# Optimization experiments

Measured on AMD Instinct MI355X. Metric: run time of the kernel, lower is better.

The kernel has to match this reference:

```python
import jax, jax.numpy as jnp
import numpy as np

N = 100000
E = 2000000
F = 64          # in_features == out_features (required by attention * h_j)
BETA = 0.5
NEG_SLOPE = 0.01  # torch F.leaky_relu default


def setup_inputs() -> dict:
    key = jax.random.key(0)
    k1, k2, k3, k4, k5, k6 = jax.random.split(key, 6)
    h = jax.random.normal(k1, (N, F), dtype=jnp.float32)
    adj = jax.random.randint(k2, (2, E), 0, N, dtype=jnp.int64)
    amount = jax.random.uniform(k3, (E,), dtype=jnp.float32)
    count = jax.random.uniform(k4, (E,), dtype=jnp.float32)
    fc_w = jax.random.normal(k5, (F, 2 * F), dtype=jnp.float32) * (1.0 / np.sqrt(2 * F))
    fc_b = jax.random.normal(k6, (F,), dtype=jnp.float32) * 0.01
    return {"h": h, "adj": adj, "amount": amount, "count": count,
            "fc_w": fc_w, "fc_b": fc_b}


def _minmax_norm(x):
    lo, hi = x.min(), x.max()
    return (x - lo) / (hi - lo + 1e-8)


def reference(h, adj, amount, count, fc_w, fc_b):
    # per-edge weight from normalized amount/count
    edge_weight = BETA * _minmax_norm(amount) + (1.0 - BETA) * _minmax_norm(count)  # [E]

    src, dst = adj[0], adj[1]
    h_i = h[src]                     # [E, F]
    h_j = h[dst]                     # [E, F]
    h_cat = jnp.concatenate([h_i, h_j], axis=1)  # [E, 2F]

    score = jnp.einsum('ef,of->eo', h_cat, fc_w) + fc_b  # [E, F_out]
    score = jnp.where(score >= 0, score, NEG_SLOPE * score)  # leaky_relu
    score = score * edge_weight[:, None]

    # softmax over ALL edges (dim 0), per feature, as in the original
    attention = jax.nn.softmax(score, axis=0)  # [E, F]

    agg = jnp.zeros_like(h).at[src].add(attention * h_j)  # scatter-add -> [N, F]
    return agg
```

## Files before the change

kernel.cpp:

```cpp
#include <hip/hip_runtime.h>
#include <hip/hip_fp16.h>
#include <math.h>

#define FDIM   64
#define NB     64
#define BSHIFT 7
#define BMASK  127
#define EPTA   16
#define CHUNKA (EPTA * 256)
#define SCH    1024
#define CAP    3072

__global__ __launch_bounds__(256) void count_mm_k(const int* __restrict__ src,
                                                  const float* __restrict__ amount,
                                                  const float* __restrict__ count,
                                                  int* __restrict__ mat,
                                                  float4* __restrict__ partial,
                                                  double* __restrict__ colsum,
                                                  int E, int nblkA, int nbkt) {
  __shared__ int lhist[1024];
  __shared__ float4 lred[4];
  for (int k = threadIdx.x; k < nbkt; k += 256) lhist[k] = 0;
  if (blockIdx.x == 0)
    for (int i = threadIdx.x; i < 1024; i += 256) colsum[i] = 0.0;
  __syncthreads();
  float amin = 3.4e38f, amax = -3.4e38f, cmin = 3.4e38f, cmax = -3.4e38f;
  int e0 = blockIdx.x * CHUNKA + threadIdx.x * EPTA;
  if (e0 + EPTA <= E) {
    #pragma unroll
    for (int q = 0; q < EPTA; q += 4) {
      int4   s4 = *(const int4*)(src + e0 + q);
      float4 a4 = *(const float4*)(amount + e0 + q);
      float4 c4 = *(const float4*)(count + e0 + q);
      atomicAdd(&lhist[s4.x >> BSHIFT], 1);
      atomicAdd(&lhist[s4.y >> BSHIFT], 1);
      atomicAdd(&lhist[s4.z >> BSHIFT], 1);
      atomicAdd(&lhist[s4.w >> BSHIFT], 1);
      amin = fminf(amin, fminf(fminf(a4.x, a4.y), fminf(a4.z, a4.w)));
      amax = fmaxf(amax, fmaxf(fmaxf(a4.x, a4.y), fmaxf(a4.z, a4.w)));
      cmin = fminf(cmin, fminf(fminf(c4.x, c4.y), fminf(c4.z, c4.w)));
      cmax = fmaxf(cmax, fmaxf(fmaxf(c4.x, c4.y), fmaxf(c4.z, c4.w)));
    }
  } else {
    for (int e = e0; e < E; e++) {
      atomicAdd(&lhist[src[e] >> BSHIFT], 1);
      float a = amount[e], c = count[e];
      amin = fminf(amin, a); amax = fmaxf(amax, a);
      cmin = fminf(cmin, c); cmax = fmaxf(cmax, c);
    }
  }
  #pragma unroll
  for (int off = 32; off; off >>= 1) {
    amin = fminf(amin, __shfl_down(amin, off));
    amax = fmaxf(amax, __shfl_down(amax, off));
    cmin = fminf(cmin, __shfl_down(cmin, off));
    cmax = fmaxf(cmax, __shfl_down(cmax, off));
  }
  if ((threadIdx.x & 63) == 0) lred[threadIdx.x >> 6] = make_float4(amin, amax, cmin, cmax);
  __syncthreads();
  for (int k = threadIdx.x; k < nbkt; k += 256)
    mat[(size_t)k * nblkA + blockIdx.x] = lhist[k];
  if (threadIdx.x == 0) {
    float4 r = lred[0];
    #pragma unroll
    for (int w = 1; w < 4; w++) {
      r.x = fminf(r.x, lred[w].x); r.y = fmaxf(r.y, lred[w].y);
      r.z = fminf(r.z, lred[w].z); r.w = fmaxf(r.w, lred[w].w);
    }
    partial[blockIdx.x] = r;
  }
}

__global__ __launch_bounds__(256) void scan1_k(const int* __restrict__ v,
                                               int* __restrict__ bsum, int M) {
  __shared__ int lds[256];
  int t = threadIdx.x, b = blockIdx.x;
  int s = 0;
  for (int i = b * SCH + t; i < min((b + 1) * SCH, M); i += 256) s += v[i];
  lds[t] = s; __syncthreads();
  for (int off = 128; off; off >>= 1) {
    if (t < off) lds[t] += lds[t + off];
    __syncthreads();
  }
  if (t == 0) bsum[b] = lds[0];
}

__global__ __launch_bounds__(256) void scan2_k(const int* __restrict__ bsum,
                                               int* __restrict__ bexcl, int nchunk,
                                               const float4* __restrict__ partial,
                                               float* __restrict__ mmf, int nb) {
  __shared__ int lds[256];
  int t = threadIdx.x;
  int running = 0;
  for (int c0 = 0; c0 < nchunk; c0 += 256) {
    int x = (c0 + t < nchunk) ? bsum[c0 + t] : 0;
    lds[t] = x; __syncthreads();
    for (int off = 1; off < 256; off <<= 1) {
      int v = (t >= off) ? lds[t - off] : 0;
      __syncthreads();
      lds[t] += v; __syncthreads();
    }
    if (c0 + t < nchunk) bexcl[c0 + t] = running + lds[t] - x;
    running += lds[255];
    __syncthreads();
  }
  float amin = 3.4e38f, amax = -3.4e38f, cmin = 3.4e38f, cmax = -3.4e38f;
  for (int i = t; i < nb; i += 256) {
    float4 p = partial[i];
    amin = fminf(amin, p.x); amax = fmaxf(amax, p.y);
    cmin = fminf(cmin, p.z); cmax = fmaxf(cmax, p.w);
  }
  #pragma unroll
  for (int off = 32; off; off >>= 1) {
    amin = fminf(amin, __shfl_down(amin, off));
    amax = fmaxf(amax, __shfl_down(amax, off));
    cmin = fminf(cmin, __shfl_down(cmin, off));
    cmax = fmaxf(cmax, __shfl_down(cmax, off));
  }
  __shared__ float4 lred[4];
  if ((t & 63) == 0) lred[t >> 6] = make_float4(amin, amax, cmin, cmax);
  __syncthreads();
  if (t == 0) {
    float4 r = lred[0];
    #pragma unroll
    for (int w = 1; w < 4; w++) {
      r.x = fminf(r.x, lred[w].x); r.y = fmaxf(r.y, lred[w].y);
      r.z = fminf(r.z, lred[w].z); r.w = fmaxf(r.w, lred[w].w);
    }
    mmf[0] = r.x; mmf[1] = r.y; mmf[2] = r.z; mmf[3] = r.w;
  }
}

__global__ __launch_bounds__(256) void scan3_k(const int* __restrict__ v,
                                               const int* __restrict__ bexcl,
                                               int* __restrict__ smat, int M) {
  __shared__ int lds[256];
  int t = threadIdx.x, b = blockIdx.x;
  int running = bexcl[b];
  for (int tile = 0; tile < SCH; tile += 256) {
    int i = b * SCH + tile + t;
    int x = (i < M) ? v[i] : 0;
    lds[t] = x; __syncthreads();
    for (int off = 1; off < 256; off <<= 1) {
      int vv = (t >= off) ? lds[t - off] : 0;
      __syncthreads();
      lds[t] += vv; __syncthreads();
    }
    if (i < M) smat[i] = running + lds[t] - x;
    running += lds[255];
    __syncthreads();
  }
}

__global__ __launch_bounds__(256) void scatter_k(const int* __restrict__ src,
                                                 const int* __restrict__ dst,
                                                 const float* __restrict__ amount,
                                                 const float* __restrict__ count,
                                                 const float* __restrict__ mmf,
                                                 const int* __restrict__ smat,
                                                 int2* __restrict__ payload,
                                                 int E, int nblkA, int nbkt) {
  __shared__ int cntb[1024];
  __shared__ int baseb[1024];
  __shared__ int sbase[1024];
  __shared__ int wsum[4];
  __shared__ int2 lpay[CHUNKA];
  __shared__ unsigned short lbkt[CHUNKA];
  const int t = threadIdx.x, blk = blockIdx.x;
  for (int k = t; k < nbkt; k += 256) {
    cntb[k] = 0;
    sbase[k] = smat[(size_t)k * nblkA + blk];
  }
  __syncthreads();
  const float amin = mmf[0], amax = mmf[1], cmin = mmf[2], cmax = mmf[3];
  const float L2E = 1.4426950408889634f;
  const float ascale = 0.5f * L2E / (amax - amin + 1e-8f);
  const float cscale = 0.5f * L2E / (cmax - cmin + 1e-8f);
  int e0 = blk * CHUNKA + t * EPTA;
  const bool full = (e0 + EPTA <= E);
  int4 S[4]; int4 D[4]; float4 A[4]; float4 C[4];
  if (full) {
    #pragma unroll
    for (int q = 0; q < 4; q++) {
      S[q] = *(const int4*)(src + e0 + 4 * q);
      D[q] = *(const int4*)(dst + e0 + 4 * q);
      A[q] = *(const float4*)(amount + e0 + 4 * q);
      C[q] = *(const float4*)(count + e0 + 4 * q);
      atomicAdd(&cntb[S[q].x >> BSHIFT], 1);
      atomicAdd(&cntb[S[q].y >> BSHIFT], 1);
      atomicAdd(&cntb[S[q].z >> BSHIFT], 1);
      atomicAdd(&cntb[S[q].w >> BSHIFT], 1);
    }
  } else {
    for (int e = e0; e < E; e++) atomicAdd(&cntb[src[e] >> BSHIFT], 1);
  }
  __syncthreads();
  {
    const int wv = t >> 6, ln = t & 63;
    int carry = 0;
    #pragma unroll
    for (int c = 0; c < 4; c++) {
      int idx = (wv << 8) + (c << 6) + ln;
      int x = (idx < nbkt) ? cntb[idx] : 0;
      int v = x;
      #pragma unroll
      for (int off = 1; off < 64; off <<= 1) {
        int u = __shfl_up(v, off);
        if (ln >= off) v += u;
      }
      if (idx < nbkt) baseb[idx] = carry + v - x;
      carry += __shfl(v, 63);
    }
    if (ln == 0) wsum[wv] = carry;
  }
  __syncthreads();
  {
    const int wv = t >> 6, ln = t & 63;
    int wpre = 0;
    #pragma unroll
    for (int i = 0; i < 4; i++) wpre += (i < wv) ? wsum[i] : 0;
    if (wpre) {
      #pragma unroll
      for (int c = 0; c < 4; c++) {
        int idx = (wv << 8) + (c << 6) + ln;
        if (idx < nbkt) baseb[idx] += wpre;
      }
    }
  }
  __syncthreads();
  for (int k = t; k < nbkt; k += 256) cntb[k] = baseb[k];
  __syncthreads();
  auto ins = [&](int s, int d, float a, float c) {
    int b = s >> BSHIFT;
    float ew = (a - amin) * ascale + (c - cmin) * cscale;
    int pos = atomicAdd(&cntb[b], 1);
    lpay[pos] = make_int2((d << 8) | (s & BMASK), __float_as_int(ew));
    lbkt[pos] = (unsigned short)b;
  };
  if (full) {
    #pragma unroll
    for (int q = 0; q < 4; q++) {
      ins(S[q].x, D[q].x, A[q].x, C[q].x);
      ins(S[q].y, D[q].y, A[q].y, C[q].y);
      ins(S[q].z, D[q].z, A[q].z, C[q].z);
      ins(S[q].w, D[q].w, A[q].w, C[q].w);
    }
  } else {
    for (int e = e0; e < E; e++) ins(src[e], dst[e], amount[e], count[e]);
  }
  __syncthreads();
  const int ned = min(CHUNKA, E - blk * CHUNKA);
  for (int i = t; i < ned; i += 256) {
    int bk = lbkt[i];
    payload[sbase[bk] + (i - baseb[bk])] = lpay[i];
  }
}

__global__ __launch_bounds__(128) void pre_gemm(const float* __restrict__ h,
                                                const float* __restrict__ fc_w,
                                                const float* __restrict__ fc_b,
                                                float* __restrict__ G1,
                                                __half2* __restrict__ P, int N) {
  __shared__ float hs[NB * FDIM];
  const int t = threadIdx.x;
  const int o = t & 63, half = t >> 6;
  float w[FDIM];
  const float* wrow = fc_w + o * 128 + half * 64;
  #pragma unroll
  for (int f = 0; f < FDIM; f += 4) {
    float4 v = *(const float4*)(wrow + f);
    w[f] = v.x; w[f + 1] = v.y; w[f + 2] = v.z; w[f + 3] = v.w;
  }
  const float bias = (half == 0) ? fc_b[o] : 0.0f;
  const int n0 = blockIdx.x * NB;
  const int nrows = min(NB, N - n0);
  for (int i = t; i < nrows * FDIM; i += 128) hs[i] = h[(size_t)n0 * FDIM + i];
  __syncthreads();
  for (int n = 0; n < nrows; n++) {
    float4 a4 = make_float4(0.f, 0.f, 0.f, 0.f);
    #pragma unroll
    for (int f = 0; f < FDIM; f += 4) {
      float4 hv = *(const float4*)(&hs[n * FDIM + f]);
      a4.x += hv.x * w[f];
      a4.y += hv.y * w[f + 1];
      a4.z += hv.z * w[f + 2];
      a4.w += hv.w * w[f + 3];
    }
    float acc = (a4.x + a4.y) + (a4.z + a4.w) + bias;
    if (half == 0) {
      G1[(size_t)(n0 + n) * FDIM + o] = acc;
    } else {
      P[(size_t)(n0 + n) * FDIM + o] =
          __halves2half2(__float2half(acc), __float2half(hs[n * FDIM + o]));
    }
  }
}

__device__ __forceinline__ float2 unpack_h2(unsigned u) {
  __half2 v = *(__half2*)&u;
  return make_float2(__low2float(v), __high2float(v));
}

__global__ __launch_bounds__(512) void fusedB_k(const int2* __restrict__ payload,
                                                const int* __restrict__ smat,
                                                const float* __restrict__ G1,
                                                const unsigned* __restrict__ P,
                                                double* __restrict__ colsum,
                                                float* __restrict__ out,
                                                int E, int nblkA, int nbkt) {
  __shared__ int2 lpay[CAP];
  __shared__ int fcnt[128];
  __shared__ int fcur[128];
  __shared__ float part[512];
  const int b = blockIdx.x;
  const int t = threadIdx.x;
  const int lane = t & 63;
  const int wv = __builtin_amdgcn_readfirstlane(t >> 6);
  const int node0 = b << BSHIFT;
  const int base = smat[(size_t)b * nblkA];
  const int end  = (b + 1 < nbkt) ? smat[(size_t)(b + 1) * nblkA] : E;
  const int nchunks = (end - base + CAP - 1) / CAP;
  const bool multi = (nchunks > 1);
  float csum = 0.0f;
  for (int c = 0; c < nchunks; c++) {
    const int cs = base + c * CAP;
    const int m = min(CAP, end - cs);
    if (t < 128) fcnt[t] = 0;
    __syncthreads();
    int2 myp0, myp1, myp2, myp3, myp4, myp5;
    {
      int i;
      i = t;            if (i < m) { myp0 = payload[cs + i]; atomicAdd(&fcnt[myp0.x & 127], 1); }
      i = t + 512;      if (i < m) { myp1 = payload[cs + i]; atomicAdd(&fcnt[myp1.x & 127], 1); }
      i = t + 1024;     if (i < m) { myp2 = payload[cs + i]; atomicAdd(&fcnt[myp2.x & 127], 1); }
      i = t + 1536;     if (i < m) { myp3 = payload[cs + i]; atomicAdd(&fcnt[myp3.x & 127], 1); }
      i = t + 2048;     if (i < m) { myp4 = payload[cs + i]; atomicAdd(&fcnt[myp4.x & 127], 1); }
      i = t + 2560;     if (i < m) { myp5 = payload[cs + i]; atomicAdd(&fcnt[myp5.x & 127], 1); }
    }
    __syncthreads();
    if (wv == 0) {
      int carry = 0;
      #pragma unroll
      for (int cc = 0; cc < 2; cc++) {
        int idx = (cc << 6) + lane;
        int x = fcnt[idx];
        int v = x;
        #pragma unroll
        for (int off = 1; off < 64; off <<= 1) {
          int u = __shfl_up(v, off);
          if (lane >= off) v += u;
        }
        fcur[idx] = carry + v - x;
        carry += __shfl(v, 63);
      }
    }
    __syncthreads();
    {
      int i;
      i = t;            if (i < m) lpay[atomicAdd(&fcur[myp0.x & 127], 1)] = myp0;
      i = t + 512;      if (i < m) lpay[atomicAdd(&fcur[myp1.x & 127], 1)] = myp1;
      i = t + 1024;     if (i < m) lpay[atomicAdd(&fcur[myp2.x & 127], 1)] = myp2;
      i = t + 1536;     if (i < m) lpay[atomicAdd(&fcur[myp3.x & 127], 1)] = myp3;
      i = t + 2048;     if (i < m) lpay[atomicAdd(&fcur[myp4.x & 127], 1)] = myp4;
      i = t + 2560;     if (i < m) lpay[atomicAdd(&fcur[myp5.x & 127], 1)] = myp5;
    }
    __syncthreads();
    const int per = (((m + 7) >> 3) + 63) & ~63;
    const int ws = wv * per;
    const int we = min(ws + per, m);
    int curnode = -1;
    bool firstf = true;
    float acc = 0.0f, g1 = 0.0f;
    auto flush_to = [&](int node) {
      if (curnode >= 0) {
        float* dp = out + (size_t)curnode * FDIM + lane;
        if (multi || firstf) { atomicAdd(dp, acc); firstf = false; }
        else *dp = acc;
      }
      curnode = node; acc = 0.0f;
      g1 = G1[(size_t)node * FDIM + lane];
    };
    for (int c0 = ws; c0 < we; c0 += 64) {
      const int mm = min(64, we - c0);
      int2 p = make_int2(0, 0);
      if (lane < mm) p = lpay[c0 + lane];
      if (mm == 64) {
        #pragma unroll 1
        for (int j = 0; j < 64; j += 16) {
          int xs[16]; float ee[16]; unsigned uu[16];
          #pragma unroll
          for (int k = 0; k < 16; k++) {
            xs[k] = __builtin_amdgcn_readlane(p.x, j + k);
            ee[k] = __int_as_float(__builtin_amdgcn_readlane(p.y, j + k));
          }
          #pragma unroll
          for (int k = 0; k < 16; k++) {
            unsigned off = (((unsigned)xs[k]) & 0xFFFFFF00u) | ((unsigned)lane << 2);
            uu[k] = *(const unsigned*)((const char*)P + off);
          }
          #pragma unroll
          for (int k = 0; k < 16; k++) {
            int node = node0 + (xs[k] & 127);
            if (node != curnode) flush_to(node);
            float2 v = unpack_h2(uu[k]);
            float sc = g1 + v.x;
            sc = fmaxf(sc, 0.01f * sc);
            float x = exp2f(sc * ee[k]);
            csum += x;
            acc += x * v.y;
          }
        }
      } else {
        for (int j = 0; j < mm; j += 16) {
          const int rem = mm - j;
          int xs[16]; float ee[16]; unsigned uu[16];
          #pragma unroll
          for (int k = 0; k < 16; k++) {
            xs[k] = __builtin_amdgcn_readlane(p.x, j + k);
            ee[k] = __int_as_float(__builtin_amdgcn_readlane(p.y, j + k));
          }
          #pragma unroll
          for (int k = 0; k < 16; k++) {
            unsigned off = (((unsigned)xs[k]) & 0xFFFFFF00u) | ((unsigned)lane << 2);
            uu[k] = *(const unsigned*)((const char*)P + off);
          }
          #pragma unroll
          for (int k = 0; k < 16; k++) {
            if (k < rem) {
              int node = node0 + (xs[k] & 127);
              if (node != curnode) flush_to(node);
              float2 v = unpack_h2(uu[k]);
              float sc = g1 + v.x;
              sc = fmaxf(sc, 0.01f * sc);
              float x = exp2f(sc * ee[k]);
              csum += x;
              acc += x * v.y;
            }
          }
        }
      }
    }
    if (curnode >= 0) atomicAdd(out + (size_t)curnode * FDIM + lane, acc);
  }
  part[t] = csum;
  __syncthreads();
  if (t < 64) {
    float tot = 0.0f;
    #pragma unroll
    for (int w = 0; w < 8; w++) tot += part[t + (w << 6)];
    atomicAdd(&colsum[t * 16], (double)tot);
  }
}

__global__ __launch_bounds__(256) void scale_k(float4* __restrict__ out4,
                                               const double* __restrict__ colsum,
                                               int total4) {
  __shared__ float rinv_s[64];
  if (threadIdx.x < 64) rinv_s[threadIdx.x] = (float)(1.0 / colsum[threadIdx.x * 16]);
  __syncthreads();
  const float4* r4 = (const float4*)rinv_s;
  int idx = blockIdx.x * blockDim.x + threadIdx.x;
  int stride = gridDim.x * blockDim.x;
  for (int i = idx; i < total4; i += stride) {
    float4 v = out4[i];
    float4 r = r4[i & 15];
    v.x *= r.x; v.y *= r.y; v.z *= r.z; v.w *= r.w;
    out4[i] = v;
  }
}

extern "C" void kernel_launch(void* const* d_in, const int* in_sizes, int n_in,
                              void* d_out, int out_size, void* d_ws, size_t ws_size,
                              hipStream_t stream) {
  const float* h      = (const float*)d_in[0];
  const int*   adj    = (const int*)d_in[1];
  const float* amount = (const float*)d_in[2];
  const float* count  = (const float*)d_in[3];
  const float* fc_w   = (const float*)d_in[4];
  const float* fc_b   = (const float*)d_in[5];
  float* out = (float*)d_out;

  const int E = in_sizes[2];
  const int N = in_sizes[0] / FDIM;
  const int* src = adj;
  const int* dst = adj + E;
  const int nbkt  = (N + BMASK) >> BSHIFT;
  const int nblkA = (E + CHUNKA - 1) / CHUNKA;
  const int M = nbkt * nblkA;
  const int nchunk = (M + SCH - 1) / SCH;

  char* ws = (char*)d_ws;
  size_t off = 0;
  auto alloc = [&](size_t bytes) { void* p = ws + off; off += (bytes + 255) & ~(size_t)255; return p; };
  float*    G1      = (float*)alloc((size_t)N * FDIM * sizeof(float));
  __half2*  P       = (__half2*)alloc((size_t)N * FDIM * sizeof(__half2));
  int2*     payload = (int2*)alloc((size_t)E * sizeof(int2));
  int*      mat     = (int*)alloc((size_t)M * sizeof(int));
  int*      smat    = (int*)alloc((size_t)M * sizeof(int));
  int*      bsum    = (int*)alloc((size_t)nchunk * sizeof(int));
  int*      bexcl   = (int*)alloc((size_t)nchunk * sizeof(int));
  float4*   mmpart  = (float4*)alloc((size_t)nblkA * sizeof(float4));
  double*   colsum  = (double*)alloc(1024 * sizeof(double));
  float*    mmf     = (float*)alloc(4 * sizeof(float));

  hipMemsetAsync(d_out, 0, (size_t)out_size * sizeof(float), stream);
  count_mm_k<<<nblkA, 256, 0, stream>>>(src, amount, count, mat, mmpart, colsum, E, nblkA, nbkt);
  scan1_k<<<nchunk, 256, 0, stream>>>(mat, bsum, M);
  scan2_k<<<1, 256, 0, stream>>>(bsum, bexcl, nchunk, mmpart, mmf, nblkA);
  scan3_k<<<nchunk, 256, 0, stream>>>(mat, bexcl, smat, M);
  scatter_k<<<nblkA, 256, 0, stream>>>(src, dst, amount, count, mmf, smat, payload, E, nblkA, nbkt);
  pre_gemm<<<(N + NB - 1) / NB, 128, 0, stream>>>(h, fc_w, fc_b, G1, P, N);
  fusedB_k<<<nbkt, 512, 0, stream>>>(payload, smat, G1, (const unsigned*)P, colsum, out, E, nblkA, nbkt);
  scale_k<<<1024, 256, 0, stream>>>((float4*)out, colsum, N * FDIM / 4);
}
```

Measured before the change: 291.3 us.

## Split each node bucket into quarters and use a persistent grid in fused aggregation

The fused aggregation kernel now splits each 128-node bucket's edge segment into four sub-ranges. These are processed as work items by a fixed grid of 2048 blocks of 256 threads, with smaller LDS chunks of 1024 edges. The aim is better load balance and occupancy than one 512-thread block per bucket (about 782 blocks), whose tails could serialize. In exchange, every flush to an output row is now an atomicAdd, since several blocks can touch the same node. There is also extra per-item sort overhead.

```diff
diff --git a/kernel.cpp b/kernel.cpp
--- a/kernel.cpp
+++ b/kernel.cpp
@@ -9,7 +9,9 @@
 #define EPTA   16
 #define CHUNKA (EPTA * 256)
 #define SCH    1024
-#define CAP    3072
+#define CAPW   1024
+#define SPLIT  4
+#define FB_GRID 2048
 
 __global__ __launch_bounds__(256) void count_mm_k(const int* __restrict__ src,
                                                   const float* __restrict__ amount,
@@ -301,132 +303,100 @@
   return make_float2(__low2float(v), __high2float(v));
 }
 
-__global__ __launch_bounds__(512) void fusedB_k(const int2* __restrict__ payload,
+__global__ __launch_bounds__(256) void fusedB_k(const int2* __restrict__ payload,
                                                 const int* __restrict__ smat,
                                                 const float* __restrict__ G1,
                                                 const unsigned* __restrict__ P,
                                                 double* __restrict__ colsum,
                                                 float* __restrict__ out,
-                                                int E, int nblkA, int nbkt) {
-  __shared__ int2 lpay[CAP];
+                                                int E, int nblkA, int nbkt,
+                                                int nitems) {
+  __shared__ int2 lpay[CAPW];
   __shared__ int fcnt[128];
   __shared__ int fcur[128];
-  __shared__ float part[512];
-  const int b = blockIdx.x;
+  __shared__ float part[256];
   const int t = threadIdx.x;
   const int lane = t & 63;
   const int wv = __builtin_amdgcn_readfirstlane(t >> 6);
-  const int node0 = b << BSHIFT;
-  const int base = smat[(size_t)b * nblkA];
-  const int end  = (b + 1 < nbkt) ? smat[(size_t)(b + 1) * nblkA] : E;
-  const int nchunks = (end - base + CAP - 1) / CAP;
-  const bool multi = (nchunks > 1);
   float csum = 0.0f;
-  for (int c = 0; c < nchunks; c++) {
-    const int cs = base + c * CAP;
-    const int m = min(CAP, end - cs);
-    if (t < 128) fcnt[t] = 0;
-    __syncthreads();
-    int2 myp0, myp1, myp2, myp3, myp4, myp5;
-    {
-      int i;
-      i = t;            if (i < m) { myp0 = payload[cs + i]; atomicAdd(&fcnt[myp0.x & 127], 1); }
-      i = t + 512;      if (i < m) { myp1 = payload[cs + i]; atomicAdd(&fcnt[myp1.x & 127], 1); }
-      i = t + 1024;     if (i < m) { myp2 = payload[cs + i]; atomicAdd(&fcnt[myp2.x & 127], 1); }
-      i = t + 1536;     if (i < m) { myp3 = payload[cs + i]; atomicAdd(&fcnt[myp3.x & 127], 1); }
-      i = t + 2048;     if (i < m) { myp4 = payload[cs + i]; atomicAdd(&fcnt[myp4.x & 127], 1); }
-      i = t + 2560;     if (i < m) { myp5 = payload[cs + i]; atomicAdd(&fcnt[myp5.x & 127], 1); }
-    }
-    __syncthreads();
-    if (wv == 0) {
-      int carry = 0;
-      #pragma unroll
-      for (int cc = 0; cc < 2; cc++) {
-        int idx = (cc << 6) + lane;
-        int x = fcnt[idx];
-        int v = x;
+  for (int w = blockIdx.x; w < nitems; w += gridDim.x) {
+    const int b = w >> 2, q = w & 3;
+    const int base = smat[(size_t)b * nblkA];
+    const int end  = (b + 1 < nbkt) ? smat[(size_t)(b + 1) * nblkA] : E;
+    const int seg  = end - base;
+    const int qlen = (seg + SPLIT - 1) / SPLIT;
+    const int is = base + q * qlen;
+    const int ie = min(is + qlen, end);
+    if (is >= ie) continue;
+    const int node0 = b << BSHIFT;
+    for (int c = is; c < ie; c += CAPW) {
+      const int m = min(CAPW, ie - c);
+      if (t < 128) fcnt[t] = 0;
+      __syncthreads();
+      int2 myp0, myp1, myp2, myp3;
+      {
+        int i;
+        i = t;        if (i < m) { myp0 = payload[c + i]; atomicAdd(&fcnt[myp0.x & 127], 1); }
+        i = t + 256;  if (i < m) { myp1 = payload[c + i]; atomicAdd(&fcnt[myp1.x & 127], 1); }
+        i = t + 512;  if (i < m) { myp2 = payload[c + i]; atomicAdd(&fcnt[myp2.x & 127], 1); }
+        i = t + 768;  if (i < m) { myp3 = payload[c + i]; atomicAdd(&fcnt[myp3.x & 127], 1); }
+      }
+      __syncthreads();
+      if (wv == 0) {
+        int carry = 0;
         #pragma unroll
-        for (int off = 1; off < 64; off <<= 1) {
-          int u = __shfl_up(v, off);
-          if (lane >= off) v += u;
+        for (int cc = 0; cc < 2; cc++) {
+          int idx = (cc << 6) + lane;
+          int x = fcnt[idx];
+          int v = x;
+          #pragma unroll
+          for (int off = 1; off < 64; off <<= 1) {
+            int u = __shfl_up(v, off);
+            if (lane >= off) v += u;
+          }
+          fcur[idx] = carry + v - x;
+          carry += __shfl(v, 63);
         }
-        fcur[idx] = carry + v - x;
-        carry += __shfl(v, 63);
       }
-    }
-    __syncthreads();
-    {
-      int i;
-      i = t;            if (i < m) lpay[atomicAdd(&fcur[myp0.x & 127], 1)] = myp0;
-      i = t + 512;      if (i < m) lpay[atomicAdd(&fcur[myp1.x & 127], 1)] = myp1;
-      i = t + 1024;     if (i < m) lpay[atomicAdd(&fcur[myp2.x & 127], 1)] = myp2;
-      i = t + 1536;     if (i < m) lpay[atomicAdd(&fcur[myp3.x & 127], 1)] = myp3;
-      i = t + 2048;     if (i < m) lpay[atomicAdd(&fcur[myp4.x & 127], 1)] = myp4;
-      i = t + 2560;     if (i < m) lpay[atomicAdd(&fcur[myp5.x & 127], 1)] = myp5;
-    }
-    __syncthreads();
-    const int per = (((m + 7) >> 3) + 63) & ~63;
-    const int ws = wv * per;
-    const int we = min(ws + per, m);
-    int curnode = -1;
-    bool firstf = true;
-    float acc = 0.0f, g1 = 0.0f;
-    auto flush_to = [&](int node) {
-      if (curnode >= 0) {
-        float* dp = out + (size_t)curnode * FDIM + lane;
-        if (multi || firstf) { atomicAdd(dp, acc); firstf = false; }
-        else *dp = acc;
+      __syncthreads();
+      {
+        int i;
+        i = t;        if (i < m) lpay[atomicAdd(&fcur[myp0.x & 127], 1)] = myp0;
+        i = t + 256;  if (i < m) lpay[atomicAdd(&fcur[myp1.x & 127], 1)] = myp1;
+        i = t + 512;  if (i < m) lpay[atomicAdd(&fcur[myp2.x & 127], 1)] = myp2;
+        i = t + 768;  if (i < m) lpay[atomicAdd(&fcur[myp3.x & 127], 1)] = myp3;
       }
-      curnode = node; acc = 0.0f;
-      g1 = G1[(size_t)node * FDIM + lane];
-    };
-    for (int c0 = ws; c0 < we; c0 += 64) {
-      const int mm = min(64, we - c0);
-      int2 p = make_int2(0, 0);
-      if (lane < mm) p = lpay[c0 + lane];
-      if (mm == 64) {
-        #pragma unroll 1
-        for (int j = 0; j < 64; j += 16) {
-          int xs[16]; float ee[16]; unsigned uu[16];
-          #pragma unroll
-          for (int k = 0; k < 16; k++) {
-            xs[k] = __builtin_amdgcn_readlane(p.x, j + k);
-            ee[k] = __int_as_float(__builtin_amdgcn_readlane(p.y, j + k));
-          }
-          #pragma unroll
-          for (int k = 0; k < 16; k++) {
-            unsigned off = (((unsigned)xs[k]) & 0xFFFFFF00u) | ((unsigned)lane << 2);
-            uu[k] = *(const unsigned*)((const char*)P + off);
-          }
-          #pragma unroll
-          for (int k = 0; k < 16; k++) {
-            int node = node0 + (xs[k] & 127);
-            if (node != curnode) flush_to(node);
-            float2 v = unpack_h2(uu[k]);
-            float sc = g1 + v.x;
-            sc = fmaxf(sc, 0.01f * sc);
-            float x = exp2f(sc * ee[k]);
-            csum += x;
-            acc += x * v.y;
-          }
-        }
-      } else {
-        for (int j = 0; j < mm; j += 16) {
-          const int rem = mm - j;
-          int xs[16]; float ee[16]; unsigned uu[16];
-          #pragma unroll
-          for (int k = 0; k < 16; k++) {
-            xs[k] = __builtin_amdgcn_readlane(p.x, j + k);
-            ee[k] = __int_as_float(__builtin_amdgcn_readlane(p.y, j + k));
-          }
-          #pragma unroll
-          for (int k = 0; k < 16; k++) {
-            unsigned off = (((unsigned)xs[k]) & 0xFFFFFF00u) | ((unsigned)lane << 2);
-            uu[k] = *(const unsigned*)((const char*)P + off);
-          }
-          #pragma unroll
-          for (int k = 0; k < 16; k++) {
-            if (k < rem) {
+      __syncthreads();
+      const int per = (((m + 3) >> 2) + 63) & ~63;
+      const int ws = wv * per;
+      const int we = min(ws + per, m);
+      int curnode = -1;
+      float acc = 0.0f, g1 = 0.0f;
+      auto flush_to = [&](int node) {
+        if (curnode >= 0) atomicAdd(out + (size_t)curnode * FDIM + lane, acc);
+        curnode = node; acc = 0.0f;
+        g1 = G1[(size_t)node * FDIM + lane];
+      };
+      for (int c0 = ws; c0 < we; c0 += 64) {
+        const int mm = min(64, we - c0);
+        int2 p = make_int2(0, 0);
+        if (lane < mm) p = lpay[c0 + lane];
+        if (mm == 64) {
+          #pragma unroll 1
+          for (int j = 0; j < 64; j += 16) {
+            int xs[16]; float ee[16]; unsigned uu[16];
+            #pragma unroll
+            for (int k = 0; k < 16; k++) {
+              xs[k] = __builtin_amdgcn_readlane(p.x, j + k);
+              ee[k] = __int_as_float(__builtin_amdgcn_readlane(p.y, j + k));
+            }
+            #pragma unroll
+            for (int k = 0; k < 16; k++) {
+              unsigned off = (((unsigned)xs[k]) & 0xFFFFFF00u) | ((unsigned)lane << 2);
+              uu[k] = *(const unsigned*)((const char*)P + off);
+            }
+            #pragma unroll
+            for (int k = 0; k < 16; k++) {
               int node = node0 + (xs[k] & 127);
               if (node != curnode) flush_to(node);
               float2 v = unpack_h2(uu[k]);
@@ -437,17 +407,43 @@
               acc += x * v.y;
             }
           }
+        } else {
+          for (int j = 0; j < mm; j += 16) {
+            const int rem = mm - j;
+            int xs[16]; float ee[16]; unsigned uu[16];
+            #pragma unroll
+            for (int k = 0; k < 16; k++) {
+              xs[k] = __builtin_amdgcn_readlane(p.x, j + k);
+              ee[k] = __int_as_float(__builtin_amdgcn_readlane(p.y, j + k));
+            }
+            #pragma unroll
+            for (int k = 0; k < 16; k++) {
+              unsigned off = (((unsigned)xs[k]) & 0xFFFFFF00u) | ((unsigned)lane << 2);
+              uu[k] = *(const unsigned*)((const char*)P + off);
+            }
+            #pragma unroll
+            for (int k = 0; k < 16; k++) {
+              if (k < rem) {
+                int node = node0 + (xs[k] & 127);
+                if (node != curnode) flush_to(node);
+                float2 v = unpack_h2(uu[k]);
+                float sc = g1 + v.x;
+                sc = fmaxf(sc, 0.01f * sc);
+                float x = exp2f(sc * ee[k]);
+                csum += x;
+                acc += x * v.y;
+              }
+            }
+          }
         }
       }
-    }
-    if (curnode >= 0) atomicAdd(out + (size_t)curnode * FDIM + lane, acc);
+      if (curnode >= 0) atomicAdd(out + (size_t)curnode * FDIM + lane, acc);
+    }
   }
   part[t] = csum;
   __syncthreads();
   if (t < 64) {
-    float tot = 0.0f;
-    #pragma unroll
-    for (int w = 0; w < 8; w++) tot += part[t + (w << 6)];
+    float tot = part[t] + part[t + 64] + part[t + 128] + part[t + 192];
     atomicAdd(&colsum[t * 16], (double)tot);
   }
 }
@@ -488,6 +484,7 @@
   const int nblkA = (E + CHUNKA - 1) / CHUNKA;
   const int M = nbkt * nblkA;
   const int nchunk = (M + SCH - 1) / SCH;
+  const int nitems = nbkt * SPLIT;
 
   char* ws = (char*)d_ws;
   size_t off = 0;
@@ -510,6 +507,6 @@
   scan3_k<<<nchunk, 256, 0, stream>>>(mat, bexcl, smat, M);
   scatter_k<<<nblkA, 256, 0, stream>>>(src, dst, amount, count, mmf, smat, payload, E, nblkA, nbkt);
   pre_gemm<<<(N + NB - 1) / NB, 128, 0, stream>>>(h, fc_w, fc_b, G1, P, N);
-  fusedB_k<<<nbkt, 512, 0, stream>>>(payload, smat, G1, (const unsigned*)P, colsum, out, E, nblkA, nbkt);
+  fusedB_k<<<FB_GRID, 256, 0, stream>>>(payload, smat, G1, (const unsigned*)P, colsum, out, E, nblkA, nbkt, nitems);
   scale_k<<<1024, 256, 0, stream>>>((float4*)out, colsum, N * FDIM / 4);
 }
```

Result: slower. 306.1 us (+5.1%).

## Replace per-block bucket matrix scan with global histogram and atomic cursors

Applied to the files above, without the earlier changes.

The per-block bucket count matrix and its three-kernel prefix scan are replaced by a global bucket histogram built with atomics. A single small scan computes bucket bases, and scatter blocks now claim output ranges through atomicAdd on per-bucket cursors. Buckets are halved to 64 nodes, and the aggregation kernel runs with 256 threads and a smaller LDS staging buffer, giving more, smaller blocks. This removes two launches and the large matrix traffic. In exchange, edge order within a bucket becomes nondeterministic, and cursor contention and more bucket entries per scatter block add cost.

```diff
diff --git a/kernel.cpp b/kernel.cpp
--- a/kernel.cpp
+++ b/kernel.cpp
@@ -4,25 +4,22 @@
 
 #define FDIM   64
 #define NB     64
-#define BSHIFT 7
-#define BMASK  127
+#define BSHIFT 6
+#define BMASK  63
+#define NBKT_AL 1792
 #define EPTA   16
 #define CHUNKA (EPTA * 256)
-#define SCH    1024
-#define CAP    3072
+#define CAP    1792
 
 __global__ __launch_bounds__(256) void count_mm_k(const int* __restrict__ src,
                                                   const float* __restrict__ amount,
                                                   const float* __restrict__ count,
-                                                  int* __restrict__ mat,
+                                                  int* __restrict__ ghist,
                                                   float4* __restrict__ partial,
-                                                  double* __restrict__ colsum,
-                                                  int E, int nblkA, int nbkt) {
-  __shared__ int lhist[1024];
+                                                  int E, int nbkt) {
+  __shared__ int lhist[NBKT_AL];
   __shared__ float4 lred[4];
   for (int k = threadIdx.x; k < nbkt; k += 256) lhist[k] = 0;
-  if (blockIdx.x == 0)
-    for (int i = threadIdx.x; i < 1024; i += 256) colsum[i] = 0.0;
   __syncthreads();
   float amin = 3.4e38f, amax = -3.4e38f, cmin = 3.4e38f, cmax = -3.4e38f;
   int e0 = blockIdx.x * CHUNKA + threadIdx.x * EPTA;
@@ -59,7 +56,7 @@
   if ((threadIdx.x & 63) == 0) lred[threadIdx.x >> 6] = make_float4(amin, amax, cmin, cmax);
   __syncthreads();
   for (int k = threadIdx.x; k < nbkt; k += 256)
-    mat[(size_t)k * nblkA + blockIdx.x] = lhist[k];
+    if (lhist[k]) atomicAdd(&ghist[k], lhist[k]);
   if (threadIdx.x == 0) {
     float4 r = lred[0];
     #pragma unroll
@@ -71,39 +68,34 @@
   }
 }
 
-__global__ __launch_bounds__(256) void scan1_k(const int* __restrict__ v,
-                                               int* __restrict__ bsum, int M) {
-  __shared__ int lds[256];
-  int t = threadIdx.x, b = blockIdx.x;
-  int s = 0;
-  for (int i = b * SCH + t; i < min((b + 1) * SCH, M); i += 256) s += v[i];
-  lds[t] = s; __syncthreads();
-  for (int off = 128; off; off >>= 1) {
-    if (t < off) lds[t] += lds[t + off];
-    __syncthreads();
-  }
-  if (t == 0) bsum[b] = lds[0];
-}
-
-__global__ __launch_bounds__(256) void scan2_k(const int* __restrict__ bsum,
-                                               int* __restrict__ bexcl, int nchunk,
+__global__ __launch_bounds__(256) void scan2_k(const int* __restrict__ ghist,
+                                               int* __restrict__ bktbase,
+                                               int* __restrict__ cursor,
+                                               int nbkt, int E,
                                                const float4* __restrict__ partial,
-                                               float* __restrict__ mmf, int nb) {
+                                               float* __restrict__ mmf, int nb,
+                                               double* __restrict__ colsum) {
   __shared__ int lds[256];
   int t = threadIdx.x;
   int running = 0;
-  for (int c0 = 0; c0 < nchunk; c0 += 256) {
-    int x = (c0 + t < nchunk) ? bsum[c0 + t] : 0;
+  for (int c0 = 0; c0 < nbkt; c0 += 256) {
+    int x = (c0 + t < nbkt) ? ghist[c0 + t] : 0;
     lds[t] = x; __syncthreads();
     for (int off = 1; off < 256; off <<= 1) {
       int v = (t >= off) ? lds[t - off] : 0;
       __syncthreads();
       lds[t] += v; __syncthreads();
     }
-    if (c0 + t < nchunk) bexcl[c0 + t] = running + lds[t] - x;
+    if (c0 + t < nbkt) {
+      int ex = running + lds[t] - x;
+      bktbase[c0 + t] = ex;
+      cursor[c0 + t] = ex;
+    }
     running += lds[255];
     __syncthreads();
   }
+  if (t == 0) bktbase[nbkt] = E;
+  for (int i = t; i < 1024; i += 256) colsum[i] = 0.0;
   float amin = 3.4e38f, amax = -3.4e38f, cmin = 3.4e38f, cmax = -3.4e38f;
   for (int i = t; i < nb; i += 256) {
     float4 p = partial[i];
@@ -131,46 +123,22 @@
   }
 }
 
-__global__ __launch_bounds__(256) void scan3_k(const int* __restrict__ v,
-                                               const int* __restrict__ bexcl,
-                                               int* __restrict__ smat, int M) {
-  __shared__ int lds[256];
-  int t = threadIdx.x, b = blockIdx.x;
-  int running = bexcl[b];
-  for (int tile = 0; tile < SCH; tile += 256) {
-    int i = b * SCH + tile + t;
-    int x = (i < M) ? v[i] : 0;
-    lds[t] = x; __syncthreads();
-    for (int off = 1; off < 256; off <<= 1) {
-      int vv = (t >= off) ? lds[t - off] : 0;
-      __syncthreads();
-      lds[t] += vv; __syncthreads();
-    }
-    if (i < M) smat[i] = running + lds[t] - x;
-    running += lds[255];
-    __syncthreads();
-  }
-}
-
 __global__ __launch_bounds__(256) void scatter_k(const int* __restrict__ src,
                                                  const int* __restrict__ dst,
                                                  const float* __restrict__ amount,
                                                  const float* __restrict__ count,
                                                  const float* __restrict__ mmf,
-                                                 const int* __restrict__ smat,
+                                                 int* __restrict__ cursor,
                                                  int2* __restrict__ payload,
-                                                 int E, int nblkA, int nbkt) {
-  __shared__ int cntb[1024];
-  __shared__ int baseb[1024];
-  __shared__ int sbase[1024];
+                                                 int E, int nbkt) {
+  __shared__ int cntb[NBKT_AL];
+  __shared__ int baseb[NBKT_AL];
+  __shared__ int sbase[NBKT_AL];
   __shared__ int wsum[4];
   __shared__ int2 lpay[CHUNKA];
   __shared__ unsigned short lbkt[CHUNKA];
   const int t = threadIdx.x, blk = blockIdx.x;
-  for (int k = t; k < nbkt; k += 256) {
-    cntb[k] = 0;
-    sbase[k] = smat[(size_t)k * nblkA + blk];
-  }
+  for (int k = t; k < nbkt; k += 256) cntb[k] = 0;
   __syncthreads();
   const float amin = mmf[0], amax = mmf[1], cmin = mmf[2], cmax = mmf[3];
   const float L2E = 1.4426950408889634f;
@@ -199,8 +167,8 @@
     const int wv = t >> 6, ln = t & 63;
     int carry = 0;
     #pragma unroll
-    for (int c = 0; c < 4; c++) {
-      int idx = (wv << 8) + (c << 6) + ln;
+    for (int c = 0; c < 7; c++) {
+      int idx = wv * 448 + (c << 6) + ln;
       int x = (idx < nbkt) ? cntb[idx] : 0;
       int v = x;
       #pragma unroll
@@ -221,14 +189,18 @@
     for (int i = 0; i < 4; i++) wpre += (i < wv) ? wsum[i] : 0;
     if (wpre) {
       #pragma unroll
-      for (int c = 0; c < 4; c++) {
-        int idx = (wv << 8) + (c << 6) + ln;
+      for (int c = 0; c < 7; c++) {
+        int idx = wv * 448 + (c << 6) + ln;
         if (idx < nbkt) baseb[idx] += wpre;
       }
     }
   }
   __syncthreads();
-  for (int k = t; k < nbkt; k += 256) cntb[k] = baseb[k];
+  for (int k = t; k < nbkt; k += 256) {
+    int cnt = cntb[k];
+    if (cnt) sbase[k] = atomicAdd(&cursor[k], cnt);
+    cntb[k] = baseb[k];
+  }
   __syncthreads();
   auto ins = [&](int s, int d, float a, float c) {
     int b = s >> BSHIFT;
@@ -301,71 +273,67 @@
   return make_float2(__low2float(v), __high2float(v));
 }
 
-__global__ __launch_bounds__(512) void fusedB_k(const int2* __restrict__ payload,
-                                                const int* __restrict__ smat,
+__global__ __launch_bounds__(256) void fusedB_k(const int2* __restrict__ payload,
+                                                const int* __restrict__ bktbase,
                                                 const float* __restrict__ G1,
                                                 const unsigned* __restrict__ P,
                                                 double* __restrict__ colsum,
                                                 float* __restrict__ out,
-                                                int E, int nblkA, int nbkt) {
+                                                int E, int nbkt) {
   __shared__ int2 lpay[CAP];
-  __shared__ int fcnt[128];
-  __shared__ int fcur[128];
-  __shared__ float part[512];
+  __shared__ int fcnt[64];
+  __shared__ int fcur[64];
+  __shared__ float part[256];
   const int b = blockIdx.x;
   const int t = threadIdx.x;
   const int lane = t & 63;
   const int wv = __builtin_amdgcn_readfirstlane(t >> 6);
   const int node0 = b << BSHIFT;
-  const int base = smat[(size_t)b * nblkA];
-  const int end  = (b + 1 < nbkt) ? smat[(size_t)(b + 1) * nblkA] : E;
+  const int base = bktbase[b];
+  const int end  = bktbase[b + 1];
   const int nchunks = (end - base + CAP - 1) / CAP;
   const bool multi = (nchunks > 1);
   float csum = 0.0f;
   for (int c = 0; c < nchunks; c++) {
     const int cs = base + c * CAP;
     const int m = min(CAP, end - cs);
-    if (t < 128) fcnt[t] = 0;
-    __syncthreads();
-    int2 myp0, myp1, myp2, myp3, myp4, myp5;
+    if (t < 64) fcnt[t] = 0;
+    __syncthreads();
+    int2 myp0, myp1, myp2, myp3, myp4, myp5, myp6;
     {
       int i;
-      i = t;            if (i < m) { myp0 = payload[cs + i]; atomicAdd(&fcnt[myp0.x & 127], 1); }
-      i = t + 512;      if (i < m) { myp1 = payload[cs + i]; atomicAdd(&fcnt[myp1.x & 127], 1); }
-      i = t + 1024;     if (i < m) { myp2 = payload[cs + i]; atomicAdd(&fcnt[myp2.x & 127], 1); }
-      i = t + 1536;     if (i < m) { myp3 = payload[cs + i]; atomicAdd(&fcnt[myp3.x & 127], 1); }
-      i = t + 2048;     if (i < m) { myp4 = payload[cs + i]; atomicAdd(&fcnt[myp4.x & 127], 1); }
-      i = t + 2560;     if (i < m) { myp5 = payload[cs + i]; atomicAdd(&fcnt[myp5.x & 127], 1); }
+      i = t;        if (i < m) { myp0 = payload[cs + i]; atomicAdd(&fcnt[myp0.x & 63], 1); }
+      i = t + 256;  if (i < m) { myp1 = payload[cs + i]; atomicAdd(&fcnt[myp1.x & 63], 1); }
+      i = t + 512;  if (i < m) { myp2 = payload[cs + i]; atomicAdd(&fcnt[myp2.x & 63], 1); }
+      i = t + 768;  if (i < m) { myp3 = payload[cs + i]; atomicAdd(&fcnt[myp3.x & 63], 1); }
+      i = t + 1024; if (i < m) { myp4 = payload[cs + i]; atomicAdd(&fcnt[myp4.x & 63], 1); }
+      i = t + 1280; if (i < m) { myp5 = payload[cs + i]; atomicAdd(&fcnt[myp5.x & 63], 1); }
+      i = t + 1536; if (i < m) { myp6 = payload[cs + i]; atomicAdd(&fcnt[myp6.x & 63], 1); }
     }
     __syncthreads();
     if (wv == 0) {
-      int carry = 0;
+      int x = fcnt[lane];
+      int v = x;
       #pragma unroll
-      for (int cc = 0; cc < 2; cc++) {
-        int idx = (cc << 6) + lane;
-        int x = fcnt[idx];
-        int v = x;
-        #pragma unroll
-        for (int off = 1; off < 64; off <<= 1) {
-          int u = __shfl_up(v, off);
-          if (lane >= off) v += u;
-        }
-        fcur[idx] = carry + v - x;
-        carry += __shfl(v, 63);
+      for (int off = 1; off < 64; off <<= 1) {
+        int u = __shfl_up(v, off);
+        if (lane >= off) v += u;
       }
+      fcur[lane] = v - x;
     }
     __syncthreads();
     {
       int i;
-      i = t;            if (i < m) lpay[atomicAdd(&fcur[myp0.x & 127], 1)] = myp0;
-      i = t + 512;      if (i < m) lpay[atomicAdd(&fcur[myp1.x & 127], 1)] = myp1;
-      i = t + 1024;     if (i < m) lpay[atomicAdd(&fcur[myp2.x & 127], 1)] = myp2;
-      i = t + 1536;     if (i < m) lpay[atomicAdd(&fcur[myp3.x & 127], 1)] = myp3;
-      i = t + 2048;     if (i < m) lpay[atomicAdd(&fcur[myp4.x & 127], 1)] = myp4;
-      i = t + 2560;     if (i < m) lpay[atomicAdd(&fcur[myp5.x & 127], 1)] = myp5;
-    }
-    __syncthreads();
-    const int per = (((m + 7) >> 3) + 63) & ~63;
+      i = t;        if (i < m) lpay[atomicAdd(&fcur[myp0.x & 63], 1)] = myp0;
+      i = t + 256;  if (i < m) lpay[atomicAdd(&fcur[myp1.x & 63], 1)] = myp1;
+      i = t + 512;  if (i < m) lpay[atomicAdd(&fcur[myp2.x & 63], 1)] = myp2;
+      i = t + 768;  if (i < m) lpay[atomicAdd(&fcur[myp3.x & 63], 1)] = myp3;
+      i = t + 1024; if (i < m) lpay[atomicAdd(&fcur[myp4.x & 63], 1)] = myp4;
+      i = t + 1280; if (i < m) lpay[atomicAdd(&fcur[myp5.x & 63], 1)] = myp5;
+      i = t + 1536; if (i < m) lpay[atomicAdd(&fcur[myp6.x & 63], 1)] = myp6;
+    }
+    __syncthreads();
+    const int per = (((m + 3) >> 2) + 63) & ~63;
     const int ws = wv * per;
     const int we = min(ws + per, m);
     int curnode = -1;
@@ -400,7 +368,7 @@
           }
           #pragma unroll
           for (int k = 0; k < 16; k++) {
-            int node = node0 + (xs[k] & 127);
+            int node = node0 + (xs[k] & 63);
             if (node != curnode) flush_to(node);
             float2 v = unpack_h2(uu[k]);
             float sc = g1 + v.x;
@@ -427,7 +395,7 @@
           #pragma unroll
           for (int k = 0; k < 16; k++) {
             if (k < rem) {
-              int node = node0 + (xs[k] & 127);
+              int node = node0 + (xs[k] & 63);
               if (node != curnode) flush_to(node);
               float2 v = unpack_h2(uu[k]);
               float sc = g1 + v.x;
@@ -441,13 +409,12 @@
       }
     }
     if (curnode >= 0) atomicAdd(out + (size_t)curnode * FDIM + lane, acc);
+    __syncthreads();
   }
   part[t] = csum;
   __syncthreads();
   if (t < 64) {
-    float tot = 0.0f;
-    #pragma unroll
-    for (int w = 0; w < 8; w++) tot += part[t + (w << 6)];
+    float tot = part[t] + part[t + 64] + part[t + 128] + part[t + 192];
     atomicAdd(&colsum[t * 16], (double)tot);
   }
 }
@@ -486,8 +453,6 @@
   const int* dst = adj + E;
   const int nbkt  = (N + BMASK) >> BSHIFT;
   const int nblkA = (E + CHUNKA - 1) / CHUNKA;
-  const int M = nbkt * nblkA;
-  const int nchunk = (M + SCH - 1) / SCH;
 
   char* ws = (char*)d_ws;
   size_t off = 0;
@@ -495,21 +460,19 @@
   float*    G1      = (float*)alloc((size_t)N * FDIM * sizeof(float));
   __half2*  P       = (__half2*)alloc((size_t)N * FDIM * sizeof(__half2));
   int2*     payload = (int2*)alloc((size_t)E * sizeof(int2));
-  int*      mat     = (int*)alloc((size_t)M * sizeof(int));
-  int*      smat    = (int*)alloc((size_t)M * sizeof(int));
-  int*      bsum    = (int*)alloc((size_t)nchunk * sizeof(int));
-  int*      bexcl   = (int*)alloc((size_t)nchunk * sizeof(int));
+  int*      ghist   = (int*)alloc((size_t)NBKT_AL * sizeof(int));
+  int*      bktbase = (int*)alloc((size_t)(NBKT_AL + 1) * sizeof(int));
+  int*      cursor  = (int*)alloc((size_t)NBKT_AL * sizeof(int));
   float4*   mmpart  = (float4*)alloc((size_t)nblkA * sizeof(float4));
   double*   colsum  = (double*)alloc(1024 * sizeof(double));
   float*    mmf     = (float*)alloc(4 * sizeof(float));
 
   hipMemsetAsync(d_out, 0, (size_t)out_size * sizeof(float), stream);
-  count_mm_k<<<nblkA, 256, 0, stream>>>(src, amount, count, mat, mmpart, colsum, E, nblkA, nbkt);
-  scan1_k<<<nchunk, 256, 0, stream>>>(mat, bsum, M);
-  scan2_k<<<1, 256, 0, stream>>>(bsum, bexcl, nchunk, mmpart, mmf, nblkA);
-  scan3_k<<<nchunk, 256, 0, stream>>>(mat, bexcl, smat, M);
-  scatter_k<<<nblkA, 256, 0, stream>>>(src, dst, amount, count, mmf, smat, payload, E, nblkA, nbkt);
+  hipMemsetAsync(ghist, 0, (size_t)nbkt * sizeof(int), stream);
+  count_mm_k<<<nblkA, 256, 0, stream>>>(src, amount, count, ghist, mmpart, E, nbkt);
+  scan2_k<<<1, 256, 0, stream>>>(ghist, bktbase, cursor, nbkt, E, mmpart, mmf, nblkA, colsum);
+  scatter_k<<<nblkA, 256, 0, stream>>>(src, dst, amount, count, mmf, cursor, payload, E, nbkt);
   pre_gemm<<<(N + NB - 1) / NB, 128, 0, stream>>>(h, fc_w, fc_b, G1, P, N);
-  fusedB_k<<<nbkt, 512, 0, stream>>>(payload, smat, G1, (const unsigned*)P, colsum, out, E, nblkA, nbkt);
+  fusedB_k<<<nbkt, 256, 0, stream>>>(payload, bktbase, G1, (const unsigned*)P, colsum, out, E, nbkt);
   scale_k<<<1024, 256, 0, stream>>>((float4*)out, colsum, N * FDIM / 4);
 }
```

New measurement: 306.4 us. +5.2%, slower.
